# Kernel optimization log

Hardware: AMD Instinct MI355X
Metric: run time of the kernel (lower is better)

## Reference

```python
import jax, jax.numpy as jnp
import numpy as np

GAMMA = 0.3        # LinearSpike surrogate-gradient slope
TIMESTEPS = 10

@jax.custom_vjp
def linear_spike(x):
    # forward: Heaviside; backward: piecewise-linear surrogate (Bellec et al. 2018)
    return (x > 0).astype(x.dtype)

def _ls_fwd(x):
    return linear_spike(x), x

def _ls_bwd(x, g):
    return (g * GAMMA * jnp.maximum(1.0 - jnp.abs(x), 0.0),)

linear_spike.defvjp(_ls_fwd, _ls_bwd)


def setup_inputs() -> dict:
    key = jax.random.key(0)
    ks = jax.random.split(key, 6)
    V, E, H, S, B = 32000, 1024, 1024, 64, 64
    return {
        "input_batch": jax.random.randint(ks[0], (S, B), 0, V),  # [seq_len, batch]
        "embedding": jax.random.normal(ks[1], (V, E), jnp.float32),
        "W1": jax.random.normal(ks[2], (H, E), jnp.float32) / np.sqrt(E).astype(np.float32),
        "b1": jnp.zeros((H,), jnp.float32),
        "W2": jax.random.normal(ks[3], (H, H), jnp.float32) / np.sqrt(H).astype(np.float32),
        "b2": jnp.zeros((H,), jnp.float32),
        "threshold": jnp.float32(1.0),
        "leak": jnp.float32(0.95),
    }


def reference(input_batch, embedding, W1, b1, W2, b2, threshold, leak):
    # Dropout masks are identity in the deterministic reference (eval mode).
    S, B = input_batch.shape
    H = W1.shape[0]
    embed = embedding[input_batch]                       # [S, B, E]
    # First Linear is constant across timesteps of a word -> hoist out of the T loop.
    h1 = jnp.einsum('sbe,he->sbh', embed, W1) + b1       # [S, B, H]

    def word_step(carry, x):                             # x: [B, H]
        def t_step(c, _):
            mem1, mem2 = c
            # LIF dynamics
            mem1 = leak * mem1 + x
            mem_thr = mem1 / threshold - 1.0
            spike = linear_spike(mem_thr)                # surrogate-grad spike
            fired = jax.lax.stop_gradient((mem_thr > 0).astype(mem1.dtype))
            mem1 = mem1 - threshold * fired              # soft reset
            # second Linear + Integrate neuron
            mem2 = mem2 + spike @ W2.T + b2
            return (mem1, mem2), None
        carry, _ = jax.lax.scan(t_step, carry, None, length=TIMESTEPS)
        return carry, None

    init = (jnp.zeros((B, H), embed.dtype), jnp.zeros((B, H), embed.dtype))
    (mem1, mem2), _ = jax.lax.scan(word_step, init, h1)
    return mem2 / B                                      # out / embed.shape[1]
```

## Files before the change

kernel.cpp:

```cpp
#include <hip/hip_runtime.h>


#define TSTEPS 10
#define SEQ    64
#define BATCH  64
#define EDIM   1024
#define HDIM   1024
#define NROW   (SEQ * BATCH)
#define KSPLIT 16

typedef unsigned short u16;
typedef __attribute__((ext_vector_type(8))) _Float16 half8;
typedef __attribute__((ext_vector_type(8))) unsigned short ushort8;
typedef __attribute__((ext_vector_type(4))) float  f32x4;

union h16 { _Float16 f; u16 u; };

__device__ __forceinline__ u16 f2h_bits(float x) {
    h16 t; t.f = (_Float16)x; return t.u;
}
__device__ __forceinline__ float h2f(u16 b) {
    h16 t; t.u = b; return (float)t.f;
}
__device__ __forceinline__ void gld16(const u16* g, u16* l) {
    __builtin_amdgcn_global_load_lds(
        (const __attribute__((address_space(1))) void*)g,
        (__attribute__((address_space(3))) void*)l, 16, 0, 0);
}

__global__ __launch_bounds__(256) void split_pack(
    const float* __restrict__ emb, const float* __restrict__ W1,
    const int* __restrict__ idx,
    u16* __restrict__ ahi, u16* __restrict__ alo, u16* __restrict__ whi)
{
    const int t = blockIdx.x * 256 + threadIdx.x;
    const int r = t >> 7;
    const int c = (t & 127) << 3;
    if (r < NROW) {
        const int srow = idx[(r & 63) * 64 + (r >> 6)];
        const float* src = emb + (size_t)srow * EDIM + c;
        float4 v0 = *(const float4*)src;
        float4 v1 = *(const float4*)(src + 4);
        float x[8] = {v0.x, v0.y, v0.z, v0.w, v1.x, v1.y, v1.z, v1.w};
        ushort8 h, l;
#pragma unroll
        for (int j = 0; j < 8; ++j) {
            u16 hh = f2h_bits(x[j]);
            h[j] = hh;
            l[j] = f2h_bits((x[j] - h2f(hh)) * 2048.0f);
        }
        *(ushort8*)(ahi + (size_t)r * EDIM + c) = h;
        *(ushort8*)(alo + (size_t)r * EDIM + c) = l;
    } else {
        const int rw = r - NROW;
        const float* src = W1 + (size_t)rw * EDIM + c;
        float4 v0 = *(const float4*)src;
        float4 v1 = *(const float4*)(src + 4);
        float x[8] = {v0.x, v0.y, v0.z, v0.w, v1.x, v1.y, v1.z, v1.w};
        ushort8 h;
#pragma unroll
        for (int j = 0; j < 8; ++j) h[j] = f2h_bits(x[j]);
        *(ushort8*)(whi + (size_t)rw * EDIM + c) = h;
    }
}

#define BM 64
#define BN 128
#define BK 32
#define NT (EDIM / BK)
#define AH 0
#define AL 2048
#define WH 4096
#define BUF 8192

__global__ __launch_bounds__(256, 3) void gemm1_lif(
    const u16* __restrict__ Ahi, const u16* __restrict__ Alo,
    const u16* __restrict__ Whi,
    const float* __restrict__ bias1,
    const float* __restrict__ pthr, const float* __restrict__ pleak,
    float* __restrict__ cnt)
{
    __shared__ float smf[12288];
    u16*   stage = (u16*)smf;
    float* ct    = smf;

    const int bid = blockIdx.x;
    const int loc = bid >> 3;
    const int by  = (bid & 7) * 8 + (loc & 7);
    const int bx  = loc >> 3;
    const int row0 = by * BM, col0 = bx * BN;

    const int tid  = threadIdx.x;
    const int wave = tid >> 6, lane = tid & 63;
    const int wn   = wave;
    const int lrow = lane & 15, kgrp = lane >> 4;

    const int srr = lane >> 2;
    const int kcs = (((lane & 3) ^ ((lane >> 3) & 3)) << 3);
    const size_t aoff = (size_t)(row0 + wave * 16 + srr) * EDIM + kcs;
    const size_t w0   = (size_t)(col0 + wave * 32 + srr) * EDIM + kcs;
    const size_t w1   = w0 + (size_t)16 * EDIM;

    f32x4 acc[4][2], acl[4][2];
    const f32x4 zero = {0.f, 0.f, 0.f, 0.f};
#pragma unroll
    for (int m = 0; m < 4; ++m)
#pragma unroll
        for (int n = 0; n < 2; ++n) { acc[m][n] = zero; acl[m][n] = zero; }

    auto STAGE = [&](int k0, int b) {
        u16* lb = stage + b * BUF;
        gld16(Ahi + aoff + k0, lb + AH + wave * 512);
        gld16(Alo + aoff + k0, lb + AL + wave * 512);
        gld16(Whi + w0 + k0, lb + WH + wave * 1024);
        gld16(Whi + w1 + k0, lb + WH + wave * 1024 + 512);
    };

    auto COMPUTE = [&](int b) {
        const u16* lb = stage + b * BUF;
        half8 ah[4], al[4], bh[2];
#pragma unroll
        for (int n = 0; n < 2; ++n) {
            const int c = wn * 32 + n * 16 + lrow;
            const int s = kgrp ^ ((c >> 1) & 3);
            bh[n] = *(const half8*)(lb + WH + c * 32 + s * 8);
        }
#pragma unroll
        for (int m = 0; m < 4; ++m) {
            const int r = m * 16 + lrow;
            const int s = kgrp ^ ((r >> 1) & 3);
            const u16* p = lb + AH + r * 32 + s * 8;
            ah[m] = *(const half8*)p;
            al[m] = *(const half8*)(p + (AL - AH));
        }
#pragma unroll
        for (int m = 0; m < 4; ++m)
#pragma unroll
            for (int n = 0; n < 2; ++n) {
                acc[m][n] = __builtin_amdgcn_mfma_f32_16x16x32_f16(ah[m], bh[n], acc[m][n], 0, 0, 0);
                acl[m][n] = __builtin_amdgcn_mfma_f32_16x16x32_f16(al[m], bh[n], acl[m][n], 0, 0, 0);
            }
    };

    STAGE(0, 0);
    STAGE(BK, 1);
    int cc = 0, cs = 2;
    for (int t = 0; t < NT - 2; ++t) {
        STAGE((t + 2) * BK, cs);
        asm volatile("s_waitcnt vmcnt(8)" ::: "memory");
        __builtin_amdgcn_s_barrier();
        __builtin_amdgcn_sched_barrier(0);
        COMPUTE(cc);
        __builtin_amdgcn_s_barrier();
        cc = (cc == 2) ? 0 : cc + 1;
        cs = (cs == 2) ? 0 : cs + 1;
    }
    asm volatile("s_waitcnt vmcnt(4)" ::: "memory");
    __builtin_amdgcn_s_barrier();
    __builtin_amdgcn_sched_barrier(0);
    COMPUTE(cc);
    cc = (cc == 2) ? 0 : cc + 1;
    asm volatile("s_waitcnt vmcnt(0)" ::: "memory");
    __builtin_amdgcn_s_barrier();
    __builtin_amdgcn_sched_barrier(0);
    COMPUTE(cc);
    __syncthreads();

#pragma unroll
    for (int n = 0; n < 2; ++n) {
        const int kc = wn * 32 + n * 16 + lrow;
#pragma unroll
        for (int m = 0; m < 4; ++m) {
            const int sb = m * 16 + kgrp * 4;
#pragma unroll
            for (int j = 0; j < 4; ++j)
                ct[kc * 66 + sb + j] = acc[m][n][j] + acl[m][n][j] * (1.0f / 2048.0f);
        }
    }
    __syncthreads();

    if (tid < BN) {
        const float thr = pthr[0];
        const float lk  = pleak[0];
        const float b1v = bias1[col0 + tid];
        const float* row = ct + tid * 66;
        float mem1 = 0.f, c = 0.f;
        for (int s = 0; s < SEQ; ++s) {
            const float x = row[s] + b1v;
#pragma unroll
            for (int t = 0; t < TSTEPS; ++t) {
                mem1 = lk * mem1 + x;
                if (mem1 > thr) { c += 1.f; mem1 -= thr; }
            }
        }
        cnt[(size_t)by * HDIM + col0 + tid] = c;
    }
}

__global__ __launch_bounds__(256) void gemm2_partial(
    const float* __restrict__ cnt,
    const float* __restrict__ W2,
    float* __restrict__ part)
{
    __shared__ float As[32][68];
    __shared__ float Bs[32][132];

    const int tid   = threadIdx.x;
    const int col0  = blockIdx.x * 128;
    const int kc    = blockIdx.y;
    const int kbase = kc * 64;

    const int lr = tid >> 3;
    const int lc = (tid & 7) * 4;
    const int tm = (tid >> 4) * 4;
    const int tn = (tid & 15) * 4;

    float acc[4][8];
#pragma unroll
    for (int i = 0; i < 4; ++i)
#pragma unroll
        for (int j = 0; j < 8; ++j) acc[i][j] = 0.f;

    for (int kt = 0; kt < 2; ++kt) {
        const int k0 = kbase + kt * 32;
#pragma unroll
        for (int p = 0; p < 2; ++p) {
            int r = p * 32 + lr;
            float4 v = *(const float4*)(cnt + (size_t)r * HDIM + k0 + lc);
            As[lc + 0][r] = v.x; As[lc + 1][r] = v.y;
            As[lc + 2][r] = v.z; As[lc + 3][r] = v.w;
        }
#pragma unroll
        for (int p = 0; p < 4; ++p) {
            int r = p * 32 + lr;
            float4 v = *(const float4*)(W2 + (size_t)(col0 + r) * HDIM + k0 + lc);
            Bs[lc + 0][r] = v.x; Bs[lc + 1][r] = v.y;
            Bs[lc + 2][r] = v.z; Bs[lc + 3][r] = v.w;
        }
        __syncthreads();
#pragma unroll 8
        for (int k = 0; k < 32; ++k) {
            float4 a   = *(const float4*)&As[k][tm];
            float4 bb0 = *(const float4*)&Bs[k][tn];
            float4 bb1 = *(const float4*)&Bs[k][tn + 64];
            float av[4] = {a.x, a.y, a.z, a.w};
            float bv[8] = {bb0.x, bb0.y, bb0.z, bb0.w, bb1.x, bb1.y, bb1.z, bb1.w};
#pragma unroll
            for (int i = 0; i < 4; ++i)
#pragma unroll
                for (int j = 0; j < 8; ++j)
                    acc[i][j] += av[i] * bv[j];
        }
        __syncthreads();
    }

#pragma unroll
    for (int i = 0; i < 4; ++i) {
        float* prow = part + (size_t)kc * (BATCH * HDIM) + (size_t)(tm + i) * HDIM + col0;
        float4 o0, o1;
        o0.x = acc[i][0]; o0.y = acc[i][1]; o0.z = acc[i][2]; o0.w = acc[i][3];
        o1.x = acc[i][4]; o1.y = acc[i][5]; o1.z = acc[i][6]; o1.w = acc[i][7];
        *(float4*)(prow + tn)      = o0;
        *(float4*)(prow + tn + 64) = o1;
    }
}

__global__ __launch_bounds__(256) void reduce_out(
    const float* __restrict__ part,
    const float* __restrict__ b2,
    float* __restrict__ out)
{
    const int i = blockIdx.x * 256 + threadIdx.x;
    float s = 0.f;
#pragma unroll
    for (int kc = 0; kc < KSPLIT; ++kc)
        s += part[(size_t)kc * (BATCH * HDIM) + i];
    const int h = i & (HDIM - 1);
    out[i] = (s + (float)(SEQ * TSTEPS) * b2[h]) * (1.0f / (float)BATCH);
}

extern "C" void kernel_launch(void* const* d_in, const int* in_sizes, int n_in,
                              void* d_out, int out_size, void* d_ws, size_t ws_size,
                              hipStream_t stream)
{
    (void)in_sizes; (void)n_in; (void)out_size; (void)ws_size;

    const int*   idx  = (const int*)d_in[0];
    const float* emb  = (const float*)d_in[1];
    const float* W1   = (const float*)d_in[2];
    const float* b1   = (const float*)d_in[3];
    const float* W2   = (const float*)d_in[4];
    const float* b2   = (const float*)d_in[5];
    const float* thr  = (const float*)d_in[6];
    const float* leak = (const float*)d_in[7];
    float* out = (float*)d_out;

    char* ws = (char*)d_ws;
    float* part = (float*)ws;
    float* cnt  = (float*)(ws + (size_t)KSPLIT * BATCH * HDIM * 4);
    u16* ahi = (u16*)(ws + (size_t)KSPLIT * BATCH * HDIM * 4 + (size_t)BATCH * HDIM * 4);
    u16* alo = ahi + (size_t)NROW * EDIM;
    u16* whi = alo + (size_t)NROW * EDIM;

    split_pack<<<dim3((NROW + HDIM) * 128 / 256), 256, 0, stream>>>(
        emb, W1, idx, ahi, alo, whi);

    gemm1_lif<<<dim3((NROW / BM) * (HDIM / BN)), 256, 0, stream>>>(
        ahi, alo, whi, b1, thr, leak, cnt);

    gemm2_partial<<<dim3(HDIM / 128, KSPLIT), 256, 0, stream>>>(cnt, W2, part);

    reduce_out<<<dim3((BATCH * HDIM) / 256), 256, 0, stream>>>(part, b2, out);
}
```

Measured before the change: 55.06 us.

## Split LIF recurrence out of GEMM1 into a separate fully-parallel kernel

```diff
diff --git a/kernel.cpp b/kernel.cpp
--- a/kernel.cpp
+++ b/kernel.cpp
@@ -73,16 +73,13 @@
 #define WH 4096
 #define BUF 8192
 
-__global__ __launch_bounds__(256, 3) void gemm1_lif(
+__global__ __launch_bounds__(256, 3) void gemm1_h1(
     const u16* __restrict__ Ahi, const u16* __restrict__ Alo,
     const u16* __restrict__ Whi,
-    const float* __restrict__ bias1,
-    const float* __restrict__ pthr, const float* __restrict__ pleak,
-    float* __restrict__ cnt)
+    float* __restrict__ h1L)
 {
     __shared__ float smf[12288];
-    u16*   stage = (u16*)smf;
-    float* ct    = smf;
+    u16* stage = (u16*)smf;
 
     const int bid = blockIdx.x;
     const int loc = bid >> 3;
@@ -164,37 +161,52 @@
     __builtin_amdgcn_s_barrier();
     __builtin_amdgcn_sched_barrier(0);
     COMPUTE(cc);
-    __syncthreads();
 
 #pragma unroll
     for (int n = 0; n < 2; ++n) {
-        const int kc = wn * 32 + n * 16 + lrow;
+        const int col = col0 + wn * 32 + n * 16 + lrow;
+        float* base = h1L + ((size_t)by * HDIM + col) * 64 + kgrp * 4;
 #pragma unroll
         for (int m = 0; m < 4; ++m) {
-            const int sb = m * 16 + kgrp * 4;
+            f32x4 v;
 #pragma unroll
             for (int j = 0; j < 4; ++j)
-                ct[kc * 66 + sb + j] = acc[m][n][j] + acl[m][n][j] * (1.0f / 2048.0f);
-        }
-    }
-    __syncthreads();
-
-    if (tid < BN) {
-        const float thr = pthr[0];
-        const float lk  = pleak[0];
-        const float b1v = bias1[col0 + tid];
-        const float* row = ct + tid * 66;
-        float mem1 = 0.f, c = 0.f;
-        for (int s = 0; s < SEQ; ++s) {
-            const float x = row[s] + b1v;
+                v[j] = acc[m][n][j] + acl[m][n][j] * (1.0f / 2048.0f);
+            *(f32x4*)(base + m * 16) = v;
+        }
+    }
+}
+
+__global__ __launch_bounds__(256) void lif_count(
+    const float* __restrict__ h1L,
+    const float* __restrict__ bias1,
+    const float* __restrict__ pthr, const float* __restrict__ pleak,
+    float* __restrict__ cnt)
+{
+    const int i = blockIdx.x * 256 + threadIdx.x;
+    const float thr = pthr[0];
+    const float lk  = pleak[0];
+    const float b1v = bias1[i & (HDIM - 1)];
+    const float4* row = (const float4*)(h1L + (size_t)i * 64);
+
+    float mem1 = 0.f, c = 0.f;
+    float4 xv = row[0];
+#pragma unroll 2
+    for (int sq = 0; sq < 16; ++sq) {
+        float4 nx = row[(sq + 1) & 15];
+        float xs[4] = {xv.x, xv.y, xv.z, xv.w};
+#pragma unroll
+        for (int u = 0; u < 4; ++u) {
+            const float x = xs[u] + b1v;
 #pragma unroll
             for (int t = 0; t < TSTEPS; ++t) {
                 mem1 = lk * mem1 + x;
                 if (mem1 > thr) { c += 1.f; mem1 -= thr; }
             }
         }
-        cnt[(size_t)by * HDIM + col0 + tid] = c;
-    }
+        xv = nx;
+    }
+    cnt[i] = c;
 }
 
 __global__ __launch_bounds__(256) void gemm2_partial(
@@ -298,15 +310,20 @@
     char* ws = (char*)d_ws;
     float* part = (float*)ws;
     float* cnt  = (float*)(ws + (size_t)KSPLIT * BATCH * HDIM * 4);
-    u16* ahi = (u16*)(ws + (size_t)KSPLIT * BATCH * HDIM * 4 + (size_t)BATCH * HDIM * 4);
+    float* h1L  = (float*)(ws + (size_t)KSPLIT * BATCH * HDIM * 4
+                              + (size_t)BATCH * HDIM * 4);
+    u16* ahi = (u16*)((char*)h1L + (size_t)NROW * HDIM * 4);
     u16* alo = ahi + (size_t)NROW * EDIM;
     u16* whi = alo + (size_t)NROW * EDIM;
 
     split_pack<<<dim3((NROW + HDIM) * 128 / 256), 256, 0, stream>>>(
         emb, W1, idx, ahi, alo, whi);
 
-    gemm1_lif<<<dim3((NROW / BM) * (HDIM / BN)), 256, 0, stream>>>(
-        ahi, alo, whi, b1, thr, leak, cnt);
+    gemm1_h1<<<dim3((NROW / BM) * (HDIM / BN)), 256, 0, stream>>>(
+        ahi, alo, whi, h1L);
+
+    lif_count<<<dim3((BATCH * HDIM) / 256), 256, 0, stream>>>(
+        h1L, b1, thr, leak, cnt);
 
     gemm2_partial<<<dim3(HDIM / 128, KSPLIT), 256, 0, stream>>>(cnt, W2, part);
 
```

Result: no change. 55.12 us (+0.1%).
